# Optimization experiments

Hardware: AMD Instinct MI355X
Metric: run time of the kernel (lower is better)

## Reference

```python
import jax, jax.numpy as jnp
import numpy as np

N = 50000; E = 600000; D = 128; NB = 20; L = 3; H = 64; NG = 512; ZMAX = 100
CUTOFF = 5.0

def setup_inputs() -> dict:
    key = jax.random.key(0)
    ks = jax.random.split(key, 32)
    inp = {}
    inp['at_no'] = jax.random.randint(ks[0], (N,), 0, ZMAX)
    inp['pos'] = jax.random.normal(ks[1], (N, 3), dtype=jnp.float32) * 3.0
    inp['edge_index'] = jax.random.randint(ks[2], (2, E), 0, N)
    inp['batch'] = jnp.sort(jax.random.randint(ks[3], (N,), 0, NG))
    def w(k, shape, fan_in):
        return (jax.random.normal(k, shape, dtype=jnp.float32) / np.sqrt(fan_in)).astype(jnp.float32)
    inp['emb'] = w(ks[4], (ZMAX, D), 1.0)
    # per-block filter net: rbf -> 3D
    inp['Wf'] = w(ks[5], (L, NB, 3 * D), NB); inp['bf'] = jnp.zeros((L, 3 * D), jnp.float32)
    # per-block message scalar MLP: D -> D -> 3D
    inp['Wm1'] = w(ks[6], (L, D, D), D);      inp['bm1'] = jnp.zeros((L, D), jnp.float32)
    inp['Wm2'] = w(ks[7], (L, D, 3 * D), D);  inp['bm2'] = jnp.zeros((L, 3 * D), jnp.float32)
    # per-block update: U, V channel-mixing on vectors; MLP 2D -> D -> 3D
    inp['U'] = w(ks[8], (L, D, D), D)
    inp['V'] = w(ks[9], (L, D, D), D)
    inp['Wu1'] = w(ks[10], (L, 2 * D, D), 2 * D); inp['bu1'] = jnp.zeros((L, D), jnp.float32)
    inp['Wu2'] = w(ks[11], (L, D, 3 * D), D);     inp['bu2'] = jnp.zeros((L, 3 * D), jnp.float32)
    # scalar output head: D -> H -> 1, graph sum
    inp['Wo1'] = w(ks[12], (D, H), D); inp['bo1'] = jnp.zeros((H,), jnp.float32)
    inp['Wo2'] = w(ks[13], (H, 1), H); inp['bo2'] = jnp.zeros((1,), jnp.float32)
    return inp

def _painn(at_no, pos, edge_index, batch, emb, Wf, bf, Wm1, bm1, Wm2, bm2,
           U, V, Wu1, bu1, Wu2, bu2, Wo1, bo1, Wo2, bo2):
    src, dst = edge_index[0], edge_index[1]
    vec = pos[dst] - pos[src]                       # [E,3]
    dist = jnp.sqrt(jnp.sum(vec * vec, axis=-1, keepdims=True) + 1e-12)  # [E,1]
    dirv = vec / dist                               # [E,3] (rsh l=1)
    n = jnp.arange(1, NB + 1, dtype=jnp.float32)
    rbf = jnp.sin(n * jnp.pi * dist / CUTOFF) / dist            # [E,NB] Bessel
    fcut = 0.5 * (jnp.cos(jnp.pi * dist / CUTOFF) + 1.0) * (dist < CUTOFF)  # [E,1]

    x = emb[at_no]                                  # [N,D]
    v = jnp.zeros((x.shape[0], 3, D), x.dtype)      # [N,3,D]

    for l in range(L):
        # ---- message ----
        filt = (rbf @ Wf[l] + bf[l]) * fcut                     # [E,3D]
        phi = jax.nn.silu(x @ Wm1[l] + bm1[l]) @ Wm2[l] + bm2[l]  # [N,3D]
        m = phi[src] * filt                                     # [E,3D]
        ds, dv1, dv2 = m[:, :D], m[:, D:2 * D], m[:, 2 * D:]
        dv = dv1[:, None, :] * dirv[:, :, None] + dv2[:, None, :] * v[src]  # [E,3,D]
        x = x + jax.ops.segment_sum(ds, dst, num_segments=N)
        v = v + jax.ops.segment_sum(dv, dst, num_segments=N)
        # ---- update ----
        Uv = jnp.einsum('ncd,de->nce', v, U[l])
        Vv = jnp.einsum('ncd,de->nce', v, V[l])
        Vn = jnp.sqrt(jnp.sum(Vv * Vv, axis=1) + 1e-8)          # [N,D]
        a = jax.nn.silu(jnp.concatenate([x, Vn], axis=-1) @ Wu1[l] + bu1[l]) @ Wu2[l] + bu2[l]
        avv, asv, ass = a[:, :D], a[:, D:2 * D], a[:, 2 * D:]
        x = x + ass + asv * jnp.sum(Uv * Vv, axis=1)
        v = v + avv[:, None, :] * Uv

    node_out = jax.nn.silu(x @ Wo1 + bo1) @ Wo2 + bo2           # [N,1]
    return jax.ops.segment_sum(node_out, batch, num_segments=NG)  # [NG,1]

def reference(at_no, pos, edge_index, batch, emb, Wf, bf, Wm1, bm1, Wm2, bm2,
              U, V, Wu1, bu1, Wu2, bu2, Wo1, bo1, Wo2, bo2):
    return _painn(at_no, pos, edge_index, batch, emb, Wf, bf, Wm1, bm1, Wm2, bm2,
                  U, V, Wu1, bu1, Wu2, bu2, Wo1, bo1, Wo2, bo2)
```

## Files before the change

### kernel.cpp

```cpp
#include <hip/hip_runtime.h>
#include <math.h>

#define NN 50000
#define NE 600000
#define ECAP 230000
#define DD 128
#define D3 384
#define NB_ 20
#define HH 64
#define NG_ 512
#define LSZ 180224

typedef short v8s __attribute__((ext_vector_type(8)));
typedef short v4sh __attribute__((ext_vector_type(4)));
typedef float v4f __attribute__((ext_vector_type(4)));

__device__ __forceinline__ float silu_f(float z) { return z / (1.0f + expf(-z)); }

__device__ __forceinline__ short f2bf(float f) {
  unsigned u = __float_as_uint(f);
  u += 0x7FFF + ((u >> 16) & 1);
  return (short)(u >> 16);
}
__device__ __forceinline__ float bf2f(short s) {
  return __uint_as_float(((unsigned)(unsigned short)s) << 16);
}
__device__ __forceinline__ void split2(float x, short& h, short& l) {
  h = f2bf(x);
  l = f2bf(x - bf2f(h));
}
__device__ __forceinline__ void split_store4(float4 f, short* hp, short* lp) {
  short h0,l0,h1,l1,h2,l2,h3,l3;
  split2(f.x,h0,l0); split2(f.y,h1,l1); split2(f.z,h2,l2); split2(f.w,h3,l3);
  v4sh hv = {h0,h1,h2,h3}, lv = {l0,l1,l2,l3};
  *(v4sh*)hp = hv; *(v4sh*)lp = lv;
}
#define MFMA3(acc, ah, al, bh, bl) \
  acc = __builtin_amdgcn_mfma_f32_16x16x32_bf16(ah, bh, acc, 0, 0, 0); \
  acc = __builtin_amdgcn_mfma_f32_16x16x32_bf16(al, bh, acc, 0, 0, 0); \
  acc = __builtin_amdgcn_mfma_f32_16x16x32_bf16(ah, bl, acc, 0, 0, 0);

__global__ void zero_f_kernel(float* __restrict__ p, long n) {
  long i = (long)blockIdx.x * blockDim.x + threadIdx.x;
  long s = (long)gridDim.x * blockDim.x;
  for (; i < n; i += s) p[i] = 0.0f;
}

__global__ void zero_i_kernel(int* __restrict__ p, long n) {
  long i = (long)blockIdx.x * blockDim.x + threadIdx.x;
  long s = (long)gridDim.x * blockDim.x;
  for (; i < n; i += s) p[i] = 0;
}

__global__ void init_x_kernel(const int* __restrict__ at_no, const float* __restrict__ emb,
                              float* __restrict__ x) {
  int i = blockIdx.x * blockDim.x + threadIdx.x;
  if (i >= NN * DD) return;
  x[i] = emb[at_no[i >> 7] * DD + (i & 127)];
}

__global__ void prep_w_kernel(const float* __restrict__ Wm1, const float* __restrict__ Wm2,
                              const float* __restrict__ U, const float* __restrict__ V,
                              const float* __restrict__ Wu1, const float* __restrict__ Wu2,
                              short* __restrict__ hi, short* __restrict__ lo) {
  int idx = blockIdx.x * 256 + threadIdx.x;
  if (idx >= 3 * LSZ) return;
  int l = idx / LSZ, r = idx % LSZ;
  const float* src; int K, N, nk;
  if (r < 16384)       { src = Wm1 + (size_t)l*16384; K = 128; N = 128; nk = r; }
  else if (r < 65536)  { src = Wm2 + (size_t)l*49152; K = 128; N = 384; nk = r - 16384; }
  else if (r < 81920)  { src = U   + (size_t)l*16384; K = 128; N = 128; nk = r - 65536; }
  else if (r < 98304)  { src = V   + (size_t)l*16384; K = 128; N = 128; nk = r - 81920; }
  else if (r < 131072) { src = Wu1 + (size_t)l*32768; K = 256; N = 128; nk = r - 98304; }
  else                 { src = Wu2 + (size_t)l*49152; K = 128; N = 384; nk = r - 131072; }
  int n = nk / K, k = nk - n * K;
  float xx = src[(size_t)k * N + n];
  short h = f2bf(xx);
  hi[idx] = h;
  lo[idx] = f2bf(xx - bf2f(h));
}

__global__ void prep_wf_kernel(const float* __restrict__ Wf, float* __restrict__ wfT) {
  int idx = blockIdx.x * 256 + threadIdx.x;
  if (idx >= 3 * 8192) return;
  int l = idx / 8192, r = idx % 8192;
  int d = r >> 6, c = r & 63;
  float v = 0.0f;
  if (c < 60) {
    int ch = c / 20, k = c % 20;
    v = Wf[(size_t)l * NB_ * D3 + (size_t)k * D3 + ch * DD + d];
  }
  wfT[(size_t)l * 8192 + d * 64 + c] = v;
}

__global__ void hist_kernel(const int* __restrict__ ei, const float* __restrict__ pos,
                            int* __restrict__ counts) {
  int e = blockIdx.x * blockDim.x + threadIdx.x;
  if (e >= NE) return;
  int s = ei[e], d = ei[NE + e];
  float dx = pos[3*d]   - pos[3*s];
  float dy = pos[3*d+1] - pos[3*s+1];
  float dz = pos[3*d+2] - pos[3*s+2];
  float d2 = dx*dx + dy*dy + dz*dz + 1e-12f;
  if (d2 < 25.0f) atomicAdd(&counts[d], 1);
}

__global__ void scan_kernel(const int* __restrict__ counts, int* __restrict__ indptr, int n) {
  __shared__ int sm[1024];
  __shared__ int carry_s;
  if (threadIdx.x == 0) carry_s = 0;
  __syncthreads();
  for (int start = 0; start < n; start += 1024) {
    int i = start + (int)threadIdx.x;
    int val = (i < n) ? counts[i] : 0;
    sm[threadIdx.x] = val;
    __syncthreads();
    for (int off = 1; off < 1024; off <<= 1) {
      int t = (threadIdx.x >= (unsigned)off) ? sm[threadIdx.x - off] : 0;
      __syncthreads();
      sm[threadIdx.x] += t;
      __syncthreads();
    }
    int c = carry_s;
    if (i < n) indptr[i] = c + sm[threadIdx.x] - val;
    __syncthreads();
    if (threadIdx.x == 0) carry_s = c + sm[1023];
    __syncthreads();
  }
  if (threadIdx.x == 0) indptr[n] = carry_s;
}

__global__ void fill_kernel(const int* __restrict__ ei, const float* __restrict__ pos,
                            const int* __restrict__ indptr, int* __restrict__ cursor,
                            int* __restrict__ srcs, float4* __restrict__ eg1,
                            float4* __restrict__ eg2) {
  int e = blockIdx.x * blockDim.x + threadIdx.x;
  if (e >= NE) return;
  int s = ei[e], d = ei[NE + e];
  float dx = pos[3*d]   - pos[3*s];
  float dy = pos[3*d+1] - pos[3*s+1];
  float dz = pos[3*d+2] - pos[3*s+2];
  float d2 = dx*dx + dy*dy + dz*dz + 1e-12f;
  if (d2 < 25.0f) {
    int p = atomicAdd(&cursor[d], 1);
    int slot = indptr[d] + p;
    float dist = sqrtf(d2);
    float inv = 1.0f / dist;
    float wang = 0.62831853071795864769f * dist;
    float s1 = __sinf(wang), c1 = __cosf(wang);
    float fc = 0.5f * (c1 + 1.0f);
    srcs[slot] = s;
    eg1[slot] = make_float4(s1, c1, fc, fc * inv);
    eg2[slot] = make_float4(dx * inv, dy * inv, dz * inv, 0.0f);
  }
}

__global__ void __launch_bounds__(512) mlp_phi_kernel(
    const float* __restrict__ x,
    const short* __restrict__ W1h, const short* __restrict__ W1l, const float* __restrict__ b1,
    const short* __restrict__ W2h, const short* __restrict__ W2l, const float* __restrict__ b2,
    float* __restrict__ C0, float* __restrict__ C1, float* __restrict__ C2, int M) {
  __shared__ short sm[4 * 32 * 136];
  #define XH_(r,c) sm[(r)*136 + (c)]
  #define XL_(r,c) sm[4352 + (r)*136 + (c)]
  #define TH_(r,c) sm[8704 + (r)*136 + (c)]
  #define TL_(r,c) sm[13056 + (r)*136 + (c)]
  int tid = threadIdx.x;
  long r0 = (long)blockIdx.x * 32;
  #pragma unroll
  for (int i = 0; i < 2; i++) {
    int lin = i*512 + tid;
    int r = lin >> 5, c4 = lin & 31;
    long row = r0 + r; if (row >= M) row = M - 1;
    float4 f = *(const float4*)(x + row*128 + c4*4);
    split_store4(f, &XH_(r, c4*4), &XL_(r, c4*4));
  }
  __syncthreads();
  int lane = tid & 63, wv = tid >> 6;
  int l15 = lane & 15, q = lane >> 4;
  {
    int n = wv*16 + l15;
    v4f acc[2] = {};
    #pragma unroll
    for (int s = 0; s < 4; s++) {
      v8s bh = *(const v8s*)(W1h + (long)n*128 + s*32 + q*8);
      v8s bl = *(const v8s*)(W1l + (long)n*128 + s*32 + q*8);
      #pragma unroll
      for (int mt = 0; mt < 2; mt++) {
        v8s ah = *(const v8s*)&XH_(mt*16 + l15, s*32 + q*8);
        v8s al = *(const v8s*)&XL_(mt*16 + l15, s*32 + q*8);
        MFMA3(acc[mt], ah, al, bh, bl);
      }
    }
    float bb = b1[n];
    #pragma unroll
    for (int mt = 0; mt < 2; mt++)
      #pragma unroll
      for (int i = 0; i < 4; i++) {
        short h, l;
        split2(silu_f(acc[mt][i] + bb), h, l);
        TH_(mt*16 + q*4 + i, n) = h;
        TL_(mt*16 + q*4 + i, n) = l;
      }
  }
  __syncthreads();
  v4f acc[2][3] = {};
  #pragma unroll
  for (int s = 0; s < 4; s++) {
    v8s ah[2], al[2];
    #pragma unroll
    for (int mt = 0; mt < 2; mt++) {
      ah[mt] = *(const v8s*)&TH_(mt*16 + l15, s*32 + q*8);
      al[mt] = *(const v8s*)&TL_(mt*16 + l15, s*32 + q*8);
    }
    #pragma unroll
    for (int j = 0; j < 3; j++) {
      int n = (wv*3 + j)*16 + l15;
      v8s bh = *(const v8s*)(W2h + (long)n*128 + s*32 + q*8);
      v8s bl = *(const v8s*)(W2l + (long)n*128 + s*32 + q*8);
      #pragma unroll
      for (int mt = 0; mt < 2; mt++) { MFMA3(acc[mt][j], ah[mt], al[mt], bh, bl); }
    }
  }
  #pragma unroll
  for (int j = 0; j < 3; j++) {
    int n = (wv*3 + j)*16 + l15;
    int sl = n >> 7, col = n & 127;
    float* C = (sl == 0) ? C0 : (sl == 1) ? C1 : C2;
    float bb = b2[n];
    #pragma unroll
    for (int mt = 0; mt < 2; mt++)
      #pragma unroll
      for (int i = 0; i < 4; i++) {
        long row = r0 + mt*16 + q*4 + i;
        if (row < M) C[row*128 + col] = acc[mt][j][i] + bb;
      }
  }
  #undef XH_
  #undef XL_
  #undef TH_
  #undef TL_
}

__global__ void __launch_bounds__(512, 3) muva_kernel(
    const float* __restrict__ phi0, const float* __restrict__ phi1,
    const float* __restrict__ phi2, const float* __restrict__ vA,
    float* __restrict__ vB, float* __restrict__ x,
    const int* __restrict__ srcs, const float4* __restrict__ eg1,
    const float4* __restrict__ eg2, const int* __restrict__ indptr,
    const float* __restrict__ wfT_l, const float* __restrict__ bf_l,
    const short* __restrict__ Uth, const short* __restrict__ Utl,
    const short* __restrict__ Vth, const short* __restrict__ Vtl,
    const short* __restrict__ W1h, const short* __restrict__ W1l, const float* __restrict__ b1,
    const short* __restrict__ W2h, const short* __restrict__ W2l, const float* __restrict__ b2) {
  __shared__ float smem[8896];
  short* sms = (short*)smem;
  #define VN(r,c)   smem[(r)*140 + (c)]
  #define XN(r,c)   smem[6720 + (r)*136 + (c)]
  #define VNH(r,c)  sms[(r)*136 + (c)]
  #define VNL(r,c)  sms[6528 + (r)*136 + (c)]
  #define CATH(r,c) sms[(r)*264 + (c)]
  #define CATL(r,c) sms[4224 + (r)*264 + (c)]
  #define T2H(r,c)  sms[8448 + (r)*136 + (c)]
  #define T2L(r,c)  sms[10624 + (r)*136 + (c)]
  const long NND = (long)NN*DD;
  int tid = threadIdx.x;
  long nb = (long)blockIdx.x * 16;
  {
    int gs = __builtin_amdgcn_readfirstlane((int)(tid >> 7));
    int d  = tid & 127;
    v4f wfv[15];
    {
      const float* wrow = wfT_l + d*64;
      #pragma unroll
      for (int j = 0; j < 15; j++) wfv[j] = *(const v4f*)(wrow + j*4);
    }
    #define WF0(k) wfv[(k)>>2][(k)&3]
    #define WF1(k) wfv[(20+(k))>>2][(20+(k))&3]
    #define WF2(k) wfv[(40+(k))>>2][(40+(k))&3]
    float bf0 = bf_l[d], bf1 = bf_l[DD + d], bf2 = bf_l[2*DD + d];
    long n0g = nb + 4*gs;
    int b0  = __builtin_amdgcn_readfirstlane(indptr[n0g]);
    int b1_ = __builtin_amdgcn_readfirstlane(indptr[n0g+1]);
    int b2_ = __builtin_amdgcn_readfirstlane(indptr[n0g+2]);
    int b3_ = __builtin_amdgcn_readfirstlane(indptr[n0g+3]);
    int b4_ = __builtin_amdgcn_readfirstlane(indptr[n0g+4]);
    int sA = 0, sB = 0, sC = 0;
    float p0A=0,p1A=0,p2A=0,w0A=0,w1A=0,w2A=0;
    float p0B=0,p1B=0,p2B=0,w0B=0,w1B=0,w2B=0;
    float p0C=0,p1C=0,p2C=0,w0C=0,w1C=0,w2C=0;
    float4 g1A={}, g2A={}, g1B={}, g2B={}, g1C={}, g2C={};
    if (b0 < b4_) {
      int s0 = srcs[b0];
      long bb = (long)s0*DD + d;
      p0A = phi0[bb]; p1A = phi1[bb]; p2A = phi2[bb];
      w0A = vA[bb]; w1A = vA[NND+bb]; w2A = vA[2*NND+bb];
      g1A = eg1[b0]; g2A = eg2[b0];
    }
    if (b0 + 1 < b4_) {
      int s1v = srcs[b0+1];
      long bb = (long)s1v*DD + d;
      p0B = phi0[bb]; p1B = phi1[bb]; p2B = phi2[bb];
      w0B = vA[bb]; w1B = vA[NND+bb]; w2B = vA[2*NND+bb];
      g1B = eg1[b0+1]; g2B = eg2[b0+1];
    }
    if (b0 + 2 < b4_) {
      int s2v = srcs[b0+2];
      long bb = (long)s2v*DD + d;
      p0C = phi0[bb]; p1C = phi1[bb]; p2C = phi2[bb];
      w0C = vA[bb]; w1C = vA[NND+bb]; w2C = vA[2*NND+bb];
      g1C = eg1[b0+2]; g2C = eg2[b0+2];
    }
    if (b0 + 3 < b4_) sA = srcs[b0+3];
    if (b0 + 4 < b4_) sB = srcs[b0+4];
    if (b0 + 5 < b4_) sC = srcs[b0+5];
    float xacc=0.f, a0=0.f, a1=0.f, a2=0.f;
    int e = b0, cur = 0, nxt = b1_;
#define SW_BODY(P0,P1,P2,W0,W1,W2, G1, G2, SS) \
    { while (e >= nxt) { int nr = 4*gs + cur; \
        XN(nr, d) = xacc; VN(nr, d) = a0; VN(16+nr, d) = a1; VN(32+nr, d) = a2; \
        xacc = 0.f; a0 = 0.f; a1 = 0.f; a2 = 0.f; \
        cur++; nxt = (cur == 1) ? b2_ : (cur == 2) ? b3_ : b4_; } \
      float c2 = 2.0f * G1.y; \
      float rkm1 = 0.f, rk = G1.x, dot0 = 0.f, dot1 = 0.f, dot2 = 0.f; \
      _Pragma("unroll") \
      for (int k = 0; k < NB_; k++) { \
        dot0 = fmaf(rk, WF0(k), dot0); \
        dot1 = fmaf(rk, WF1(k), dot1); \
        dot2 = fmaf(rk, WF2(k), dot2); \
        float rn = fmaf(c2, rk, -rkm1); \
        rkm1 = rk; rk = rn; } \
      xacc = fmaf(P0, bf0*G1.z + G1.w*dot0, xacc); \
      float m1 = P1 * (bf1*G1.z + G1.w*dot1); \
      float m2 = P2 * (bf2*G1.z + G1.w*dot2); \
      a0 = fmaf(m1, G2.x, fmaf(m2, W0, a0)); \
      a1 = fmaf(m1, G2.y, fmaf(m2, W1, a1)); \
      a2 = fmaf(m1, G2.z, fmaf(m2, W2, a2)); \
      if (e + 3 < b4_) { \
        long bb = (long)SS*DD + d; \
        P0 = phi0[bb]; P1 = phi1[bb]; P2 = phi2[bb]; \
        W0 = vA[bb]; W1 = vA[NND+bb]; W2 = vA[2*NND+bb]; \
        G1 = eg1[e+3]; G2 = eg2[e+3]; } \
      if (e + 6 < b4_) SS = srcs[e+6]; \
      ++e; }
    while (e < b4_) {
      SW_BODY(p0A,p1A,p2A,w0A,w1A,w2A, g1A, g2A, sA)
      if (e >= b4_) break;
      SW_BODY(p0B,p1B,p2B,w0B,w1B,w2B, g1B, g2B, sB)
      if (e >= b4_) break;
      SW_BODY(p0C,p1C,p2C,w0C,w1C,w2C, g1C, g2C, sC)
    }
#undef SW_BODY
    #undef WF0
    #undef WF1
    #undef WF2
    while (cur < 4) {
      int nr = 4*gs + cur;
      XN(nr, d) = xacc; VN(nr, d) = a0; VN(16+nr, d) = a1; VN(32+nr, d) = a2;
      xacc = 0.f; a0 = 0.f; a1 = 0.f; a2 = 0.f;
      cur++;
    }
  }
  int lane = tid & 63, wv = tid >> 6;
  int l15 = lane & 15, q = lane >> 4;
  int dc = wv*16 + l15;
  float4 vb4[3]; float4 xb4;
  {
    int ch = tid * 3;
    #pragma unroll
    for (int j = 0; j < 3; j++) {
      int r = (ch + j) >> 5, c4 = (ch + j) & 31;
      vb4[j] = *(const float4*)(vA + (long)(r >> 4)*NND + (nb + (r & 15))*DD + c4*4);
    }
    int r = tid >> 5, c4 = tid & 31;
    xb4 = *(const float4*)(x + (nb + r)*DD + c4*4);
  }
  float vbold[4][3];
  #pragma unroll
  for (int i = 0; i < 4; i++)
    #pragma unroll
    for (int c = 0; c < 3; c++)
      vbold[i][c] = vA[(long)c*NND + (nb + q*4 + i)*DD + dc];
  __syncthreads();
  float voldd[4][3];
  #pragma unroll
  for (int i = 0; i < 4; i++)
    #pragma unroll
    for (int c = 0; c < 3; c++) voldd[i][c] = VN(c*16 + q*4 + i, dc);
  float4 cf[3];
  {
    int ch = tid * 3;
    #pragma unroll
    for (int j = 0; j < 3; j++) {
      int r = (ch + j) >> 5, c4 = (ch + j) & 31;
      float4 t = *(const float4*)&VN(r, c4*4);
      cf[j] = make_float4(vb4[j].x + t.x, vb4[j].y + t.y, vb4[j].z + t.z, vb4[j].w + t.w);
    }
    int r = tid >> 5, c4 = tid & 31;
    float4 t = *(float4*)&XN(r, c4*4);
    *(float4*)&XN(r, c4*4) = make_float4(xb4.x + t.x, xb4.y + t.y, xb4.z + t.z, xb4.w + t.w);
  }
  __syncthreads();
  {
    int ch = tid * 3;
    #pragma unroll
    for (int j = 0; j < 3; j++) {
      int r = (ch + j) >> 5, c4 = (ch + j) & 31;
      split_store4(cf[j], &VNH(r, c4*4), &VNL(r, c4*4));
    }
  }
  __syncthreads();
  v4f aU[3] = {}, aV[3] = {};
  #pragma unroll
  for (int s = 0; s < 4; s++) {
    long boff = (long)dc*128 + s*32 + q*8;
    v8s buh = *(const v8s*)(Uth + boff);
    v8s bul = *(const v8s*)(Utl + boff);
    v8s bvh = *(const v8s*)(Vth + boff);
    v8s bvl = *(const v8s*)(Vtl + boff);
    #pragma unroll
    for (int c = 0; c < 3; c++) {
      v8s ah = *(const v8s*)&VNH(c*16 + l15, s*32 + q*8);
      v8s al = *(const v8s*)&VNL(c*16 + l15, s*32 + q*8);
      MFMA3(aU[c], ah, al, buh, bul);
      MFMA3(aV[c], ah, al, bvh, bvl);
    }
  }
  float sreg[4], vn2[4];
  #pragma unroll
  for (int i = 0; i < 4; i++) {
    sreg[i] = aU[0][i]*aV[0][i] + aU[1][i]*aV[1][i] + aU[2][i]*aV[2][i];
    vn2[i]  = aV[0][i]*aV[0][i] + aV[1][i]*aV[1][i] + aV[2][i]*aV[2][i];
  }
  __syncthreads();
  {
    int r = tid >> 5, c4 = tid & 31;
    float4 f = *(const float4*)&XN(r, c4*4);
    split_store4(f, &CATH(r, c4*4), &CATL(r, c4*4));
  }
  #pragma unroll
  for (int i = 0; i < 4; i++) {
    short h, l;
    split2(sqrtf(vn2[i] + 1e-8f), h, l);
    CATH(q*4 + i, 128 + dc) = h;
    CATL(q*4 + i, 128 + dc) = l;
  }
  __syncthreads();
  {
    v4f acc = {};
    #pragma unroll
    for (int s = 0; s < 8; s++) {
      v8s ah = *(const v8s*)&CATH(l15, s*32 + q*8);
      v8s al = *(const v8s*)&CATL(l15, s*32 + q*8);
      v8s bh = *(const v8s*)(W1h + (long)dc*256 + s*32 + q*8);
      v8s bl = *(const v8s*)(W1l + (long)dc*256 + s*32 + q*8);
      MFMA3(acc, ah, al, bh, bl);
    }
    float bb = b1[dc];
    #pragma unroll
    for (int i = 0; i < 4; i++) {
      short h, l;
      split2(silu_f(acc[i] + bb), h, l);
      T2H(q*4 + i, dc) = h;
      T2L(q*4 + i, dc) = l;
    }
  }
  __syncthreads();
  {
    v4f acc[3] = {};
    #pragma unroll
    for (int s = 0; s < 4; s++) {
      v8s ah = *(const v8s*)&T2H(l15, s*32 + q*8);
      v8s al = *(const v8s*)&T2L(l15, s*32 + q*8);
      #pragma unroll
      for (int g = 0; g < 3; g++) {
        int n = g*128 + dc;
        v8s bh = *(const v8s*)(W2h + (long)n*128 + s*32 + q*8);
        v8s bl = *(const v8s*)(W2l + (long)n*128 + s*32 + q*8);
        MFMA3(acc[g], ah, al, bh, bl);
      }
    }
    float bavv = b2[dc], basv = b2[128 + dc], bass = b2[256 + dc];
    #pragma unroll
    for (int i = 0; i < 4; i++) {
      int lr = q*4 + i;
      long row = nb + lr;
      float avv = acc[0][i] + bavv;
      float asv = acc[1][i] + basv;
      float ass = acc[2][i] + bass;
      x[row*DD + dc] = XN(lr, dc) + ass + asv * sreg[i];
      #pragma unroll
      for (int c = 0; c < 3; c++)
        vB[(long)c*NND + row*DD + dc] = fmaf(avv, aU[c][i], voldd[i][c] + vbold[i][c]);
    }
  }
  #undef VN
  #undef XN
  #undef VNH
  #undef VNL
  #undef CATH
  #undef CATL
  #undef T2H
  #undef T2L
}

__global__ void __launch_bounds__(256) out_kernel(
    const float* __restrict__ x, const float* __restrict__ Wo1,
    const float* __restrict__ bo1, const float* __restrict__ Wo2,
    const float* __restrict__ bo2, const int* __restrict__ batch,
    float* __restrict__ out) {
  __shared__ float xs[4][132];
  int tid = threadIdx.x;
  long n0 = (long)blockIdx.x * 4;
  if (tid < 128) {
    int r = tid >> 5, c4 = tid & 31;
    *(float4*)&xs[r][c4*4] = *(const float4*)(x + (n0 + r)*128 + c4*4);
  }
  __syncthreads();
  int wv = tid >> 6, t = tid & 63;
  float acc = bo1[t];
  #pragma unroll 16
  for (int k = 0; k < DD; k++) acc = fmaf(xs[wv][k], Wo1[k*HH + t], acc);
  float val = silu_f(acc) * Wo2[t];
  #pragma unroll
  for (int off = 32; off > 0; off >>= 1) val += __shfl_down(val, off);
  if (t == 0) atomicAdd(&out[batch[n0 + wv]], val + bo2[0]);
}

extern "C" void kernel_launch(void* const* d_in, const int* in_sizes, int n_in,
                              void* d_out, int out_size, void* d_ws, size_t ws_size,
                              hipStream_t stream) {
  const int*   at_no = (const int*)d_in[0];
  const float* pos   = (const float*)d_in[1];
  const int*   ei    = (const int*)d_in[2];
  const int*   batch = (const int*)d_in[3];
  const float* emb   = (const float*)d_in[4];
  const float* Wf    = (const float*)d_in[5];
  const float* bfp   = (const float*)d_in[6];
  const float* Wm1   = (const float*)d_in[7];
  const float* bm1   = (const float*)d_in[8];
  const float* Wm2   = (const float*)d_in[9];
  const float* bm2   = (const float*)d_in[10];
  const float* U     = (const float*)d_in[11];
  const float* V     = (const float*)d_in[12];
  const float* Wu1   = (const float*)d_in[13];
  const float* bu1   = (const float*)d_in[14];
  const float* Wu2   = (const float*)d_in[15];
  const float* bu2   = (const float*)d_in[16];
  const float* Wo1   = (const float*)d_in[17];
  const float* bo1   = (const float*)d_in[18];
  const float* Wo2   = (const float*)d_in[19];
  const float* bo2   = (const float*)d_in[20];
  float* out = (float*)d_out;

  char* w = (char*)d_ws;
  auto alloc = [&](size_t bytes) -> void* {
    void* p = (void*)w;
    w += (bytes + 255) & ~(size_t)255;
    return p;
  };
  float*  x      = (float*)alloc(sizeof(float)*(size_t)NN*DD);
  float*  v_a    = (float*)alloc(sizeof(float)*(size_t)NN*D3);
  float*  v_b    = (float*)alloc(sizeof(float)*(size_t)NN*D3);
  float*  t1     = (float*)alloc(sizeof(float)*(size_t)NN*DD);
  float*  phiS   = (float*)alloc(sizeof(float)*(size_t)NN*DD);
  float*  phi0   = (float*)alloc(sizeof(float)*(size_t)NN*DD);
  short*  wbh    = (short*)alloc(sizeof(short)*(size_t)3*LSZ);
  short*  wbl    = (short*)alloc(sizeof(short)*(size_t)3*LSZ);
  int*    srcs   = (int*)alloc(sizeof(int)*(size_t)ECAP);
  float4* eg1    = (float4*)alloc(sizeof(float4)*(size_t)ECAP);
  float4* eg2    = (float4*)alloc(sizeof(float4)*(size_t)ECAP);
  int*    indptr = (int*)alloc(sizeof(int)*((size_t)NN+1));
  int*    counts = (int*)alloc(sizeof(int)*(size_t)NN);
  float*  wfT    = (float*)alloc(sizeof(float)*(size_t)3*8192);

  if ((size_t)(w - (char*)d_ws) > ws_size) {
    zero_f_kernel<<<2, 256, 0, stream>>>(out, NG_);
    return;
  }

  zero_f_kernel<<<2048, 256, 0, stream>>>(v_a, (long)NN*D3);
  zero_f_kernel<<<2, 256, 0, stream>>>(out, NG_);
  zero_i_kernel<<<64, 256, 0, stream>>>(counts, NN);
  init_x_kernel<<<(NN*DD + 255)/256, 256, 0, stream>>>(at_no, emb, x);
  prep_w_kernel<<<(3*LSZ + 255)/256, 256, 0, stream>>>(Wm1, Wm2, U, V, Wu1, Wu2, wbh, wbl);
  prep_wf_kernel<<<96, 256, 0, stream>>>(Wf, wfT);
  hist_kernel<<<(NE + 255)/256, 256, 0, stream>>>(ei, pos, counts);
  scan_kernel<<<1, 1024, 0, stream>>>(counts, indptr, NN);
  zero_i_kernel<<<64, 256, 0, stream>>>(counts, NN);
  fill_kernel<<<(NE + 255)/256, 256, 0, stream>>>(ei, pos, indptr, counts, srcs, eg1, eg2);

  const int MB = (NN + 31) / 32;
  float* vcur = v_a;
  float* vnext = v_b;
  for (int l = 0; l < 3; l++) {
    const float* wfT_l = wfT + (size_t)l*8192;
    const float* bf_l  = bfp + (size_t)l*D3;
    const float* bm1_l = bm1 + (size_t)l*DD;
    const float* bm2_l = bm2 + (size_t)l*D3;
    const float* bu1_l = bu1 + (size_t)l*DD;
    const float* bu2_l = bu2 + (size_t)l*D3;
    const short* Lh = wbh + (size_t)l*LSZ;
    const short* Ll = wbl + (size_t)l*LSZ;
    const short* Wm1h = Lh,          *Wm1L = Ll;
    const short* Wm2h = Lh + 16384,  *Wm2L = Ll + 16384;
    const short* Uh   = Lh + 65536,  *UL   = Ll + 65536;
    const short* Vh   = Lh + 81920,  *VL   = Ll + 81920;
    const short* Wu1h = Lh + 98304,  *Wu1L = Ll + 98304;
    const short* Wu2h = Lh + 131072, *Wu2L = Ll + 131072;

    mlp_phi_kernel<<<MB, 512, 0, stream>>>(x, Wm1h, Wm1L, bm1_l, Wm2h, Wm2L, bm2_l,
                                           phi0, phiS, t1, NN);
    muva_kernel<<<NN/16, 512, 0, stream>>>(phi0, phiS, t1, vcur, vnext, x,
                                           srcs, eg1, eg2, indptr, wfT_l, bf_l,
                                           Uh, UL, Vh, VL,
                                           Wu1h, Wu1L, bu1_l, Wu2h, Wu2L, bu2_l);

    float* tmp = vcur; vcur = vnext; vnext = tmp;
  }

  out_kernel<<<NN/4, 256, 0, stream>>>(x, Wo1, bo1, Wo2, bo2, batch, out);

  (void)in_sizes; (void)n_in; (void)out_size; (void)ws_size;
}
```

Baseline: 1.405 ms.

## Split edge sweep from node update into separate kernels with a delta buffer

Unfuses the edge-message aggregation from the node update. A new per-node sweep kernel (128 threads, one node per block) writes the aggregated vector deltas to a global buffer and adds the scalar messages to x in place. The update kernel then reads v plus the delta and writes v in place, which removes the ping-pong v buffer and the shared-memory staging of the sweep. The aim is better occupancy and load balance for the gather-heavy sweep, at the cost of an extra NN*3*D write and read through global memory and one more launch per layer.

```diff
diff --git a/kernel.cpp b/kernel.cpp
--- a/kernel.cpp
+++ b/kernel.cpp
@@ -242,86 +242,50 @@
   #undef TL_
 }
 
-__global__ void __launch_bounds__(512, 3) muva_kernel(
+__global__ void __launch_bounds__(128, 8) sweep_kernel(
     const float* __restrict__ phi0, const float* __restrict__ phi1,
     const float* __restrict__ phi2, const float* __restrict__ vA,
-    float* __restrict__ vB, float* __restrict__ x,
+    float* __restrict__ x, float* __restrict__ vd,
     const int* __restrict__ srcs, const float4* __restrict__ eg1,
     const float4* __restrict__ eg2, const int* __restrict__ indptr,
-    const float* __restrict__ wfT_l, const float* __restrict__ bf_l,
-    const short* __restrict__ Uth, const short* __restrict__ Utl,
-    const short* __restrict__ Vth, const short* __restrict__ Vtl,
-    const short* __restrict__ W1h, const short* __restrict__ W1l, const float* __restrict__ b1,
-    const short* __restrict__ W2h, const short* __restrict__ W2l, const float* __restrict__ b2) {
-  __shared__ float smem[8896];
-  short* sms = (short*)smem;
-  #define VN(r,c)   smem[(r)*140 + (c)]
-  #define XN(r,c)   smem[6720 + (r)*136 + (c)]
-  #define VNH(r,c)  sms[(r)*136 + (c)]
-  #define VNL(r,c)  sms[6528 + (r)*136 + (c)]
-  #define CATH(r,c) sms[(r)*264 + (c)]
-  #define CATL(r,c) sms[4224 + (r)*264 + (c)]
-  #define T2H(r,c)  sms[8448 + (r)*136 + (c)]
-  #define T2L(r,c)  sms[10624 + (r)*136 + (c)]
+    const float* __restrict__ wfT_l, const float* __restrict__ bf_l) {
   const long NND = (long)NN*DD;
-  int tid = threadIdx.x;
-  long nb = (long)blockIdx.x * 16;
-  {
-    int gs = __builtin_amdgcn_readfirstlane((int)(tid >> 7));
-    int d  = tid & 127;
-    v4f wfv[15];
-    {
-      const float* wrow = wfT_l + d*64;
-      #pragma unroll
-      for (int j = 0; j < 15; j++) wfv[j] = *(const v4f*)(wrow + j*4);
-    }
-    #define WF0(k) wfv[(k)>>2][(k)&3]
-    #define WF1(k) wfv[(20+(k))>>2][(20+(k))&3]
-    #define WF2(k) wfv[(40+(k))>>2][(40+(k))&3]
-    float bf0 = bf_l[d], bf1 = bf_l[DD + d], bf2 = bf_l[2*DD + d];
-    long n0g = nb + 4*gs;
-    int b0  = __builtin_amdgcn_readfirstlane(indptr[n0g]);
-    int b1_ = __builtin_amdgcn_readfirstlane(indptr[n0g+1]);
-    int b2_ = __builtin_amdgcn_readfirstlane(indptr[n0g+2]);
-    int b3_ = __builtin_amdgcn_readfirstlane(indptr[n0g+3]);
-    int b4_ = __builtin_amdgcn_readfirstlane(indptr[n0g+4]);
-    int sA = 0, sB = 0, sC = 0;
-    float p0A=0,p1A=0,p2A=0,w0A=0,w1A=0,w2A=0;
-    float p0B=0,p1B=0,p2B=0,w0B=0,w1B=0,w2B=0;
-    float p0C=0,p1C=0,p2C=0,w0C=0,w1C=0,w2C=0;
-    float4 g1A={}, g2A={}, g1B={}, g2B={}, g1C={}, g2C={};
-    if (b0 < b4_) {
-      int s0 = srcs[b0];
-      long bb = (long)s0*DD + d;
-      p0A = phi0[bb]; p1A = phi1[bb]; p2A = phi2[bb];
-      w0A = vA[bb]; w1A = vA[NND+bb]; w2A = vA[2*NND+bb];
-      g1A = eg1[b0]; g2A = eg2[b0];
-    }
-    if (b0 + 1 < b4_) {
-      int s1v = srcs[b0+1];
-      long bb = (long)s1v*DD + d;
-      p0B = phi0[bb]; p1B = phi1[bb]; p2B = phi2[bb];
-      w0B = vA[bb]; w1B = vA[NND+bb]; w2B = vA[2*NND+bb];
-      g1B = eg1[b0+1]; g2B = eg2[b0+1];
-    }
-    if (b0 + 2 < b4_) {
-      int s2v = srcs[b0+2];
-      long bb = (long)s2v*DD + d;
-      p0C = phi0[bb]; p1C = phi1[bb]; p2C = phi2[bb];
-      w0C = vA[bb]; w1C = vA[NND+bb]; w2C = vA[2*NND+bb];
-      g1C = eg1[b0+2]; g2C = eg2[b0+2];
-    }
-    if (b0 + 3 < b4_) sA = srcs[b0+3];
-    if (b0 + 4 < b4_) sB = srcs[b0+4];
-    if (b0 + 5 < b4_) sC = srcs[b0+5];
-    float xacc=0.f, a0=0.f, a1=0.f, a2=0.f;
-    int e = b0, cur = 0, nxt = b1_;
+  int n = blockIdx.x;
+  int d = threadIdx.x;
+  v4f wfv[15];
+  {
+    const float* wrow = wfT_l + d*64;
+    #pragma unroll
+    for (int j = 0; j < 15; j++) wfv[j] = *(const v4f*)(wrow + j*4);
+  }
+  #define WF0(k) wfv[(k)>>2][(k)&3]
+  #define WF1(k) wfv[(20+(k))>>2][(20+(k))&3]
+  #define WF2(k) wfv[(40+(k))>>2][(40+(k))&3]
+  float bf0 = bf_l[d], bf1 = bf_l[DD + d], bf2 = bf_l[2*DD + d];
+  int e = indptr[n], end = indptr[n+1];
+  int sA = 0, sB = 0;
+  float p0A=0,p1A=0,p2A=0,w0A=0,w1A=0,w2A=0;
+  float p0B=0,p1B=0,p2B=0,w0B=0,w1B=0,w2B=0;
+  float4 g1A={}, g2A={}, g1B={}, g2B={};
+  if (e < end) {
+    int s0 = srcs[e];
+    long bb = (long)s0*DD + d;
+    p0A = phi0[bb]; p1A = phi1[bb]; p2A = phi2[bb];
+    w0A = vA[bb]; w1A = vA[NND+bb]; w2A = vA[2*NND+bb];
+    g1A = eg1[e]; g2A = eg2[e];
+  }
+  if (e + 1 < end) {
+    int s1v = srcs[e+1];
+    long bb = (long)s1v*DD + d;
+    p0B = phi0[bb]; p1B = phi1[bb]; p2B = phi2[bb];
+    w0B = vA[bb]; w1B = vA[NND+bb]; w2B = vA[2*NND+bb];
+    g1B = eg1[e+1]; g2B = eg2[e+1];
+  }
+  if (e + 2 < end) sA = srcs[e+2];
+  if (e + 3 < end) sB = srcs[e+3];
+  float xacc=0.f, a0=0.f, a1=0.f, a2=0.f;
 #define SW_BODY(P0,P1,P2,W0,W1,W2, G1, G2, SS) \
-    { while (e >= nxt) { int nr = 4*gs + cur; \
-        XN(nr, d) = xacc; VN(nr, d) = a0; VN(16+nr, d) = a1; VN(32+nr, d) = a2; \
-        xacc = 0.f; a0 = 0.f; a1 = 0.f; a2 = 0.f; \
-        cur++; nxt = (cur == 1) ? b2_ : (cur == 2) ? b3_ : b4_; } \
-      float c2 = 2.0f * G1.y; \
+    { float c2 = 2.0f * G1.y; \
       float rkm1 = 0.f, rk = G1.x, dot0 = 0.f, dot1 = 0.f, dot2 = 0.f; \
       _Pragma("unroll") \
       for (int k = 0; k < NB_; k++) { \
@@ -336,71 +300,72 @@
       a0 = fmaf(m1, G2.x, fmaf(m2, W0, a0)); \
       a1 = fmaf(m1, G2.y, fmaf(m2, W1, a1)); \
       a2 = fmaf(m1, G2.z, fmaf(m2, W2, a2)); \
-      if (e + 3 < b4_) { \
+      if (e + 2 < end) { \
         long bb = (long)SS*DD + d; \
         P0 = phi0[bb]; P1 = phi1[bb]; P2 = phi2[bb]; \
         W0 = vA[bb]; W1 = vA[NND+bb]; W2 = vA[2*NND+bb]; \
-        G1 = eg1[e+3]; G2 = eg2[e+3]; } \
-      if (e + 6 < b4_) SS = srcs[e+6]; \
+        G1 = eg1[e+2]; G2 = eg2[e+2]; } \
+      if (e + 4 < end) SS = srcs[e+4]; \
       ++e; }
-    while (e < b4_) {
-      SW_BODY(p0A,p1A,p2A,w0A,w1A,w2A, g1A, g2A, sA)
-      if (e >= b4_) break;
-      SW_BODY(p0B,p1B,p2B,w0B,w1B,w2B, g1B, g2B, sB)
-      if (e >= b4_) break;
-      SW_BODY(p0C,p1C,p2C,w0C,w1C,w2C, g1C, g2C, sC)
-    }
+  while (e < end) {
+    SW_BODY(p0A,p1A,p2A,w0A,w1A,w2A, g1A, g2A, sA)
+    if (e >= end) break;
+    SW_BODY(p0B,p1B,p2B,w0B,w1B,w2B, g1B, g2B, sB)
+  }
 #undef SW_BODY
-    #undef WF0
-    #undef WF1
-    #undef WF2
-    while (cur < 4) {
-      int nr = 4*gs + cur;
-      XN(nr, d) = xacc; VN(nr, d) = a0; VN(16+nr, d) = a1; VN(32+nr, d) = a2;
-      xacc = 0.f; a0 = 0.f; a1 = 0.f; a2 = 0.f;
-      cur++;
-    }
-  }
+  #undef WF0
+  #undef WF1
+  #undef WF2
+  long b = (long)n*DD + d;
+  x[b] += xacc;
+  vd[b]         = a0;
+  vd[NND + b]   = a1;
+  vd[2*NND + b] = a2;
+}
+
+__global__ void __launch_bounds__(512, 3) muva_kernel(
+    const float* __restrict__ vd, float* __restrict__ vA, float* __restrict__ x,
+    const short* __restrict__ Uth, const short* __restrict__ Utl,
+    const short* __restrict__ Vth, const short* __restrict__ Vtl,
+    const short* __restrict__ W1h, const short* __restrict__ W1l, const float* __restrict__ b1,
+    const short* __restrict__ W2h, const short* __restrict__ W2l, const float* __restrict__ b2) {
+  __shared__ float smem[8896];
+  short* sms = (short*)smem;
+  #define XN(r,c)   smem[6720 + (r)*136 + (c)]
+  #define VNH(r,c)  sms[(r)*136 + (c)]
+  #define VNL(r,c)  sms[6528 + (r)*136 + (c)]
+  #define CATH(r,c) sms[(r)*264 + (c)]
+  #define CATL(r,c) sms[4224 + (r)*264 + (c)]
+  #define T2H(r,c)  sms[8448 + (r)*136 + (c)]
+  #define T2L(r,c)  sms[10624 + (r)*136 + (c)]
+  const long NND = (long)NN*DD;
+  int tid = threadIdx.x;
+  long nb = (long)blockIdx.x * 16;
   int lane = tid & 63, wv = tid >> 6;
   int l15 = lane & 15, q = lane >> 4;
   int dc = wv*16 + l15;
-  float4 vb4[3]; float4 xb4;
+  float4 cf[3];
   {
     int ch = tid * 3;
     #pragma unroll
     for (int j = 0; j < 3; j++) {
       int r = (ch + j) >> 5, c4 = (ch + j) & 31;
-      vb4[j] = *(const float4*)(vA + (long)(r >> 4)*NND + (nb + (r & 15))*DD + c4*4);
+      long off = (long)(r >> 4)*NND + (nb + (r & 15))*DD + c4*4;
+      float4 bs = *(const float4*)(vA + off);
+      float4 dl = *(const float4*)(vd + off);
+      cf[j] = make_float4(bs.x + dl.x, bs.y + dl.y, bs.z + dl.z, bs.w + dl.w);
     }
     int r = tid >> 5, c4 = tid & 31;
-    xb4 = *(const float4*)(x + (nb + r)*DD + c4*4);
-  }
-  float vbold[4][3];
+    *(float4*)&XN(r, c4*4) = *(const float4*)(x + (nb + r)*DD + c4*4);
+  }
+  float vold[4][3];
   #pragma unroll
   for (int i = 0; i < 4; i++)
     #pragma unroll
-    for (int c = 0; c < 3; c++)
-      vbold[i][c] = vA[(long)c*NND + (nb + q*4 + i)*DD + dc];
-  __syncthreads();
-  float voldd[4][3];
-  #pragma unroll
-  for (int i = 0; i < 4; i++)
-    #pragma unroll
-    for (int c = 0; c < 3; c++) voldd[i][c] = VN(c*16 + q*4 + i, dc);
-  float4 cf[3];
-  {
-    int ch = tid * 3;
-    #pragma unroll
-    for (int j = 0; j < 3; j++) {
-      int r = (ch + j) >> 5, c4 = (ch + j) & 31;
-      float4 t = *(const float4*)&VN(r, c4*4);
-      cf[j] = make_float4(vb4[j].x + t.x, vb4[j].y + t.y, vb4[j].z + t.z, vb4[j].w + t.w);
-    }
-    int r = tid >> 5, c4 = tid & 31;
-    float4 t = *(float4*)&XN(r, c4*4);
-    *(float4*)&XN(r, c4*4) = make_float4(xb4.x + t.x, xb4.y + t.y, xb4.z + t.z, xb4.w + t.w);
-  }
-  __syncthreads();
+    for (int c = 0; c < 3; c++) {
+      long off = (long)c*NND + (nb + q*4 + i)*DD + dc;
+      vold[i][c] = vA[off] + vd[off];
+    }
   {
     int ch = tid * 3;
     #pragma unroll
@@ -491,10 +456,9 @@
       x[row*DD + dc] = XN(lr, dc) + ass + asv * sreg[i];
       #pragma unroll
       for (int c = 0; c < 3; c++)
-        vB[(long)c*NND + row*DD + dc] = fmaf(avv, aU[c][i], voldd[i][c] + vbold[i][c]);
-    }
-  }
-  #undef VN
+        vA[(long)c*NND + row*DD + dc] = fmaf(avv, aU[c][i], vold[i][c]);
+    }
+  }
   #undef XN
   #undef VNH
   #undef VNL
@@ -560,8 +524,8 @@
     return p;
   };
   float*  x      = (float*)alloc(sizeof(float)*(size_t)NN*DD);
-  float*  v_a    = (float*)alloc(sizeof(float)*(size_t)NN*D3);
-  float*  v_b    = (float*)alloc(sizeof(float)*(size_t)NN*D3);
+  float*  v      = (float*)alloc(sizeof(float)*(size_t)NN*D3);
+  float*  vd     = (float*)alloc(sizeof(float)*(size_t)NN*D3);
   float*  t1     = (float*)alloc(sizeof(float)*(size_t)NN*DD);
   float*  phiS   = (float*)alloc(sizeof(float)*(size_t)NN*DD);
   float*  phi0   = (float*)alloc(sizeof(float)*(size_t)NN*DD);
@@ -579,7 +543,7 @@
     return;
   }
 
-  zero_f_kernel<<<2048, 256, 0, stream>>>(v_a, (long)NN*D3);
+  zero_f_kernel<<<2048, 256, 0, stream>>>(v, (long)NN*D3);
   zero_f_kernel<<<2, 256, 0, stream>>>(out, NG_);
   zero_i_kernel<<<64, 256, 0, stream>>>(counts, NN);
   init_x_kernel<<<(NN*DD + 255)/256, 256, 0, stream>>>(at_no, emb, x);
@@ -591,8 +555,6 @@
   fill_kernel<<<(NE + 255)/256, 256, 0, stream>>>(ei, pos, indptr, counts, srcs, eg1, eg2);
 
   const int MB = (NN + 31) / 32;
-  float* vcur = v_a;
-  float* vnext = v_b;
   for (int l = 0; l < 3; l++) {
     const float* wfT_l = wfT + (size_t)l*8192;
     const float* bf_l  = bfp + (size_t)l*D3;
@@ -611,12 +573,11 @@
 
     mlp_phi_kernel<<<MB, 512, 0, stream>>>(x, Wm1h, Wm1L, bm1_l, Wm2h, Wm2L, bm2_l,
                                            phi0, phiS, t1, NN);
-    muva_kernel<<<NN/16, 512, 0, stream>>>(phi0, phiS, t1, vcur, vnext, x,
-                                           srcs, eg1, eg2, indptr, wfT_l, bf_l,
+    sweep_kernel<<<NN, 128, 0, stream>>>(phi0, phiS, t1, v, x, vd,
+                                         srcs, eg1, eg2, indptr, wfT_l, bf_l);
+    muva_kernel<<<NN/16, 512, 0, stream>>>(vd, v, x,
                                            Uh, UL, Vh, VL,
                                            Wu1h, Wu1L, bu1_l, Wu2h, Wu2L, bu2_l);
-
-    float* tmp = vcur; vcur = vnext; vnext = tmp;
   }
 
   out_kernel<<<NN/4, 256, 0, stream>>>(x, Wo1, bo1, Wo2, bo2, batch, out);
```

Result: slower. 3.691 ms (+162.6%).
